# Kernel optimization log

Measured on AMD Instinct MI355X. Metric: run time of the kernel, lower is better.

Reference implementation:

```python
import jax, jax.numpy as jnp
import numpy as np

NEG_INF = -1000000000.0
B, N, D, H, L, DFF = 4, 1024, 512, 8, 6, 2048
DH = D // H
R2 = 10.0 ** 2  # locality_radius^2
EPS = 1e-5


def setup_inputs() -> dict:
    key = jax.random.key(0)
    ks = jax.random.split(key, 16)
    s = 0.02
    inp = {
        "tokens": jax.random.normal(ks[0], (B, N, D), jnp.float32),
        "xy": jax.random.uniform(ks[1], (B, N, 2), jnp.float32) * 100.0,
        "Wq": jax.random.normal(ks[2], (L, D, D), jnp.float32) * s,
        "Wk": jax.random.normal(ks[3], (L, D, D), jnp.float32) * s,
        "Wv": jax.random.normal(ks[4], (L, D, D), jnp.float32) * s,
        "Wo": jax.random.normal(ks[5], (L, D, D), jnp.float32) * s,
        "bo": jnp.zeros((L, D), jnp.float32),
        "W1": jax.random.normal(ks[6], (L, D, DFF), jnp.float32) * s,
        "b1": jnp.zeros((L, DFF), jnp.float32),
        "W2": jax.random.normal(ks[7], (L, DFF, D), jnp.float32) * s,
        "b2": jnp.zeros((L, D), jnp.float32),
        "g1": jnp.ones((L, D), jnp.float32),
        "be1": jnp.zeros((L, D), jnp.float32),
        "g2": jnp.ones((L, D), jnp.float32),
        "be2": jnp.zeros((L, D), jnp.float32),
        "gf": jnp.ones((D,), jnp.float32),
        "bf": jnp.zeros((D,), jnp.float32),
        "alive": jax.random.randint(ks[8], (B, N), 0, 2, dtype=jnp.int32),
        "species": jax.random.randint(ks[9], (B, N), 0, 3, dtype=jnp.int32),
        "n_agents": 512,
    }
    return inp


def _ln(x, g, b):
    m = jnp.mean(x, axis=-1, keepdims=True)
    v = jnp.mean((x - m) ** 2, axis=-1, keepdims=True)
    return (x - m) * jax.lax.rsqrt(v + EPS) * g + b


def _build_bias(alive, xy, species, dtype):
    # (B,1,N,N) additive bias, broadcast over heads (original repeats per head)
    af = alive.astype(dtype)
    bias = (1.0 - af)[:, None, None, :] * NEG_INF  # dead keys
    d2 = jnp.sum((xy[:, :, None, :] - xy[:, None, :, :]) ** 2, axis=-1)  # (B,N,N)
    bias = bias + jnp.where(d2 > R2, NEG_INF, 0.0)[:, None, :, :]
    ia = species < 2
    ip = species == 2
    ct = (ia[:, :, None] & ip[:, None, :]) | (ip[:, :, None] & ia[:, None, :])
    bias = bias + jnp.where(ct, NEG_INF, 0.0)[:, None, :, :]
    return bias


def reference(tokens, xy, Wq, Wk, Wv, Wo, bo, W1, b1, W2, b2,
              g1, be1, g2, be2, gf, bf, alive, species, n_agents):
    bias = _build_bias(alive, xy, species, tokens.dtype)
    scale = np.float32(np.sqrt(DH))
    x = tokens
    for l in range(L):
        h = _ln(x, g1[l], be1[l])
        q = (h @ Wq[l]).reshape(B, N, H, DH)
        k = (h @ Wk[l]).reshape(B, N, H, DH)
        v = (h @ Wv[l]).reshape(B, N, H, DH)
        scores = jnp.einsum('bihd,bjhd->bhij', q, k) / scale + bias
        w = jax.nn.softmax(scores, axis=-1)
        o = jnp.einsum('bhij,bjhd->bihd', w, v).reshape(B, N, D)
        x = x + (o @ Wo[l] + bo[l])
        h2 = _ln(x, g2[l], be2[l])
        ff = jax.nn.gelu(h2 @ W1[l] + b1[l], approximate=False) @ W2[l] + b2[l]
        x = x + ff
    return _ln(x, gf, bf)
```

## Files before the change

kernel.cpp:

```cpp
#include <hip/hip_runtime.h>
#include <math.h>

namespace {

constexpr int B = 4, N = 1024, D = 512, H = 8, DHd = 64, L = 6, DFFd = 2048;
constexpr int M = B * N;
constexpr int QKVS = 3 * D;
constexpr float NEG = -1000000000.0f;
constexpr float R2c = 100.0f;

typedef __attribute__((ext_vector_type(8))) short bf16x8;
typedef __attribute__((ext_vector_type(4))) float f32x4;
typedef __attribute__((ext_vector_type(16))) float f32x16;

__device__ __forceinline__ short f2bf(float f) {
  union { float f; unsigned u; } c; c.f = f;
  unsigned r = (c.u + 0x7fffu + ((c.u >> 16) & 1u)) >> 16;
  return (short)r;
}

__device__ __forceinline__ float gelu_f(float x) {
  return 0.5f * x * (1.0f + erff(x * 0.70710678118654752f));
}

__global__ __launch_bounds__(256) void bias_kernel(
    const float* __restrict__ xy, const int* __restrict__ alive,
    const int* __restrict__ species, float* __restrict__ bias)
{
  int j = blockIdx.x * 256 + threadIdx.x;
  int i = blockIdx.y;
  int b = blockIdx.z;
  float xi = xy[((size_t)b * N + i) * 2 + 0];
  float yi = xy[((size_t)b * N + i) * 2 + 1];
  float xj = xy[((size_t)b * N + j) * 2 + 0];
  float yj = xy[((size_t)b * N + j) * 2 + 1];
  float dx = xi - xj, dy = yi - yj;
  float d2 = dx * dx + dy * dy;
  float bv = 0.0f;
  if (alive[b * N + j] == 0) bv += NEG;
  if (d2 > R2c) bv += NEG;
  int si = species[b * N + i], sj = species[b * N + j];
  bool ia = si < 2, ip = si == 2, ja = sj < 2, jp = sj == 2;
  if ((ia && jp) || (ip && ja)) bv += NEG;
  bias[((size_t)b * N + i) * N + j] = bv;
}

__global__ __launch_bounds__(256) void wprep_kernel(
    const float* __restrict__ src, short* __restrict__ dst,
    int K, int Nc, size_t srcLS, size_t dstLS)
{
  __shared__ float t[32][33];
  int k0 = blockIdx.x * 32, n0 = blockIdx.y * 32;
  src += (size_t)blockIdx.z * srcLS;
  dst += (size_t)blockIdx.z * dstLS;
  int r = threadIdx.x >> 5, c = threadIdx.x & 31;
#pragma unroll
  for (int i = 0; i < 4; ++i)
    t[r + i * 8][c] = src[(size_t)(k0 + r + i * 8) * Nc + n0 + c];
  __syncthreads();
#pragma unroll
  for (int i = 0; i < 4; ++i)
    dst[(size_t)(n0 + r + i * 8) * K + k0 + c] = f2bf(t[c][r + i * 8]);
}

__global__ __launch_bounds__(64) void ln_kernel(
    const float* __restrict__ x, const float* __restrict__ g,
    const float* __restrict__ be, float* __restrict__ outf,
    short* __restrict__ outb)
{
  int row = blockIdx.x;
  int tid = threadIdx.x;
  const float* xr = x + (size_t)row * D;
  float v[8];
  float sum = 0.f;
#pragma unroll
  for (int i = 0; i < 8; ++i) { v[i] = xr[tid + i * 64]; sum += v[i]; }
#pragma unroll
  for (int off = 32; off > 0; off >>= 1) sum += __shfl_down(sum, off);
  sum = __shfl(sum, 0);
  float mean = sum * (1.0f / D);
  float vs = 0.f;
#pragma unroll
  for (int i = 0; i < 8; ++i) { float d = v[i] - mean; vs += d * d; }
#pragma unroll
  for (int off = 32; off > 0; off >>= 1) vs += __shfl_down(vs, off);
  vs = __shfl(vs, 0);
  float rstd = rsqrtf(vs * (1.0f / D) + 1e-5f);
#pragma unroll
  for (int i = 0; i < 8; ++i) {
    int c = tid + i * 64;
    float o = (v[i] - mean) * rstd * g[c] + be[c];
    if (outb) outb[(size_t)row * D + c] = f2bf(o);
    else      outf[(size_t)row * D + c] = o;
  }
}

__global__ __launch_bounds__(256, 2) void gemm_sk_kernel(
    const short* __restrict__ A, const short* __restrict__ Bt,
    const float* __restrict__ bvec, float* __restrict__ Cf,
    short* __restrict__ Cb, int K, int Nc, int mode)
{
  __shared__ __align__(16) char smem[4 * 17408];
  const int bm = blockIdx.y * 64, bn = blockIdx.x * 64;
  const int t = threadIdx.x, wave = t >> 6, lane = t & 63;
  const int half = lane >> 5;
  const int l32 = lane & 31;
  const int srow4 = lane >> 2, sseg4 = lane & 3;

  char* slot = smem + wave * 17408;
  const int kw0 = wave * (K >> 2);
  const int nch = K >> 7;

  const short* Ab = A + (size_t)(bm + srow4) * K + kw0 + sseg4 * 8;
  const short* Bb = Bt + (size_t)(bn + srow4) * K + kw0 + sseg4 * 8;

  auto issue = [&](int p, int kc) {
    char* ab = slot + p * 8192;
    char* bb = slot + p * 8192 + 4096;
#pragma unroll
    for (int i = 0; i < 4; ++i) {
      __builtin_amdgcn_global_load_lds(
          (const __attribute__((address_space(1))) void*)(Ab + (size_t)i * 16 * K + kc),
          (__attribute__((address_space(3))) void*)(ab + i * 1024), 16, 0, 0);
    }
#pragma unroll
    for (int i = 0; i < 4; ++i) {
      __builtin_amdgcn_global_load_lds(
          (const __attribute__((address_space(1))) void*)(Bb + (size_t)i * 16 * K + kc),
          (__attribute__((address_space(3))) void*)(bb + i * 1024), 16, 0, 0);
    }
  };

  f32x16 acc[2][2];
#pragma unroll
  for (int i = 0; i < 2; ++i)
#pragma unroll
    for (int j = 0; j < 2; ++j)
#pragma unroll
      for (int r = 0; r < 16; ++r) acc[i][j][r] = 0.f;

  issue(0, 0);
  for (int c = 0; c < nch; ++c) {
    const int p = c & 1;
    if (c + 1 < nch) {
      issue(p ^ 1, (c + 1) * 32);
      asm volatile("s_waitcnt vmcnt(%0)" :: "i"(8) : "memory");
    } else {
      asm volatile("s_waitcnt vmcnt(0)" ::: "memory");
    }
    const short* As = (const short*)(slot + p * 8192);
    const short* Bs = (const short*)(slot + p * 8192 + 4096);
#pragma unroll
    for (int ks = 0; ks < 2; ++ks) {
      bf16x8 a0 = *(const bf16x8*)&As[(l32) * 32 + ks * 16 + half * 8];
      bf16x8 a1 = *(const bf16x8*)&As[(32 + l32) * 32 + ks * 16 + half * 8];
      bf16x8 b0 = *(const bf16x8*)&Bs[(l32) * 32 + ks * 16 + half * 8];
      bf16x8 b1 = *(const bf16x8*)&Bs[(32 + l32) * 32 + ks * 16 + half * 8];
      acc[0][0] = __builtin_amdgcn_mfma_f32_32x32x16_bf16(a0, b0, acc[0][0], 0, 0, 0);
      acc[0][1] = __builtin_amdgcn_mfma_f32_32x32x16_bf16(a0, b1, acc[0][1], 0, 0, 0);
      acc[1][0] = __builtin_amdgcn_mfma_f32_32x32x16_bf16(a1, b0, acc[1][0], 0, 0, 0);
      acc[1][1] = __builtin_amdgcn_mfma_f32_32x32x16_bf16(a1, b1, acc[1][1], 0, 0, 0);
    }
  }

  float* red = (float*)slot;
#pragma unroll
  for (int ti = 0; ti < 2; ++ti)
#pragma unroll
    for (int tj = 0; tj < 2; ++tj)
#pragma unroll
      for (int r = 0; r < 16; ++r) {
        int row = ti * 32 + (r & 3) + 8 * (r >> 2) + 4 * half;
        red[row * 68 + tj * 32 + l32] = acc[ti][tj][r];
      }
  __syncthreads();

  const int row = t >> 2, cs = (t & 3) * 16;
  const size_t orow = (size_t)(bm + row) * Nc + bn + cs;
#pragma unroll
  for (int u = 0; u < 4; ++u) {
    float4 s0 = *(const float4*)((const float*)(smem + 0 * 17408) + row * 68 + cs + u * 4);
    float4 s1 = *(const float4*)((const float*)(smem + 1 * 17408) + row * 68 + cs + u * 4);
    float4 s2 = *(const float4*)((const float*)(smem + 2 * 17408) + row * 68 + cs + u * 4);
    float4 s3 = *(const float4*)((const float*)(smem + 3 * 17408) + row * 68 + cs + u * 4);
    float o0 = s0.x + s1.x + s2.x + s3.x;
    float o1 = s0.y + s1.y + s2.y + s3.y;
    float o2 = s0.z + s1.z + s2.z + s3.z;
    float o3 = s0.w + s1.w + s2.w + s3.w;
    const int col = bn + cs + u * 4;
    if (mode == 0) {
      short4 w = {f2bf(o0), f2bf(o1), f2bf(o2), f2bf(o3)};
      *(short4*)&Cb[orow + u * 4] = w;
    } else if (mode == 1) {
      float4 bv = *(const float4*)&bvec[col];
      float4 rv = *(const float4*)&Cf[orow + u * 4];
      float4 w = {o0 + bv.x + rv.x, o1 + bv.y + rv.y, o2 + bv.z + rv.z, o3 + bv.w + rv.w};
      *(float4*)&Cf[orow + u * 4] = w;
    } else {
      float4 bv = *(const float4*)&bvec[col];
      short4 w = {f2bf(gelu_f(o0 + bv.x)), f2bf(gelu_f(o1 + bv.y)),
                  f2bf(gelu_f(o2 + bv.z)), f2bf(gelu_f(o3 + bv.w))};
      *(short4*)&Cb[orow + u * 4] = w;
    }
  }
}

__global__ __launch_bounds__(256) void attn_mfma_kernel(
    const short* __restrict__ qkv, const float* __restrict__ bias,
    short* __restrict__ o)
{
  constexpr int LDR = 72;
  __shared__ __align__(16) short Qs[64 * LDR];
  __shared__ __align__(16) short Ks[2][64 * LDR];
  __shared__ __align__(16) short Vt[2][64 * LDR];
  __shared__ __align__(16) short Ps[4 * 16 * LDR];

  const int q0 = blockIdx.x * 64;
  const int hh = blockIdx.y;
  const int b  = blockIdx.z;
  const int t  = threadIdx.x;
  const int wave = t >> 6;
  const int lane = t & 63;
  const int quad = lane >> 4;
  const int ln16 = lane & 15;
  const int srow = t >> 2, sseg = t & 3;

  {
    const short* qb = qkv + (size_t)(b * N + q0 + srow) * QKVS + hh * 64 + sseg * 16;
    *(bf16x8*)&Qs[srow * LDR + sseg * 16] = *(const bf16x8*)qb;
    *(bf16x8*)&Qs[srow * LDR + sseg * 16 + 8] = *(const bf16x8*)(qb + 8);
  }
  __syncthreads();

  const int qrow = wave * 16 + ln16;
  const bf16x8 qf0 = *(const bf16x8*)&Qs[qrow * LDR + quad * 8];
  const bf16x8 qf1 = *(const bf16x8*)&Qs[qrow * LDR + 32 + quad * 8];

  float m_run = -1e30f, l_run = 0.f;
  f32x4 Oacc[4];
#pragma unroll
  for (int dt = 0; dt < 4; ++dt) Oacc[dt] = (f32x4){0.f, 0.f, 0.f, 0.f};

  short* Psw = Ps + wave * 16 * LDR;
  const float* brow = bias + (size_t)(b * N + q0 + wave * 16 + ln16) * N;
  const short* kb0 = qkv + (size_t)b * N * QKVS + 512 + hh * 64 + sseg * 16;
  const short* vb0 = qkv + (size_t)b * N * QKVS + 1024 + hh * 64 + sseg * 16;

  bf16x8 k0r = *(const bf16x8*)(kb0 + (size_t)srow * QKVS);
  bf16x8 k1r = *(const bf16x8*)(kb0 + (size_t)srow * QKVS + 8);
  bf16x8 v0r = *(const bf16x8*)(vb0 + (size_t)srow * QKVS);
  bf16x8 v1r = *(const bf16x8*)(vb0 + (size_t)srow * QKVS + 8);
  float4 b4[4];
#pragma unroll
  for (int ks = 0; ks < 4; ++ks)
    b4[ks] = *(const float4*)&brow[ks * 16 + quad * 4];

  for (int kt = 0; kt < 16; ++kt) {
    const int p = kt & 1;
    *(bf16x8*)&Ks[p][srow * LDR + sseg * 16] = k0r;
    *(bf16x8*)&Ks[p][srow * LDR + sseg * 16 + 8] = k1r;
#pragma unroll
    for (int e = 0; e < 8; ++e) {
      Vt[p][(sseg * 16 + e) * LDR + srow] = v0r[e];
      Vt[p][(sseg * 16 + 8 + e) * LDR + srow] = v1r[e];
    }
    const int k0n = (kt + 1 < 16) ? (kt + 1) * 64 : 0;
    bf16x8 nk0 = *(const bf16x8*)(kb0 + (size_t)(k0n + srow) * QKVS);
    bf16x8 nk1 = *(const bf16x8*)(kb0 + (size_t)(k0n + srow) * QKVS + 8);
    bf16x8 nv0 = *(const bf16x8*)(vb0 + (size_t)(k0n + srow) * QKVS);
    bf16x8 nv1 = *(const bf16x8*)(vb0 + (size_t)(k0n + srow) * QKVS + 8);
    float4 bcur[4] = {b4[0], b4[1], b4[2], b4[3]};
#pragma unroll
    for (int ks = 0; ks < 4; ++ks)
      b4[ks] = *(const float4*)&brow[k0n + ks * 16 + quad * 4];
    asm volatile("s_waitcnt lgkmcnt(0)\n\ts_barrier" ::: "memory");

    float sv[4][4];
#pragma unroll
    for (int ks = 0; ks < 4; ++ks) {
      bf16x8 a0 = *(const bf16x8*)&Ks[p][(ks * 16 + ln16) * LDR + quad * 8];
      bf16x8 a1 = *(const bf16x8*)&Ks[p][(ks * 16 + ln16) * LDR + 32 + quad * 8];
      f32x4 z = (f32x4){0.f, 0.f, 0.f, 0.f};
      z = __builtin_amdgcn_mfma_f32_16x16x32_bf16(a0, qf0, z, 0, 0, 0);
      z = __builtin_amdgcn_mfma_f32_16x16x32_bf16(a1, qf1, z, 0, 0, 0);
#pragma unroll
      for (int r = 0; r < 4; ++r)
        sv[ks][r] = z[r] * 0.125f + (&bcur[ks].x)[r];
    }

    float mt = sv[0][0];
#pragma unroll
    for (int ks = 0; ks < 4; ++ks)
#pragma unroll
      for (int r = 0; r < 4; ++r) mt = fmaxf(mt, sv[ks][r]);
    mt = fmaxf(mt, __shfl_xor(mt, 16));
    mt = fmaxf(mt, __shfl_xor(mt, 32));
    const float m_new = fmaxf(m_run, mt);
    const float alpha = __expf(m_run - m_new);
    m_run = m_new;
    float rs = 0.f;
    float pv[4][4];
#pragma unroll
    for (int ks = 0; ks < 4; ++ks)
#pragma unroll
      for (int r = 0; r < 4; ++r) {
        float e = __expf(sv[ks][r] - m_new);
        pv[ks][r] = e;
        rs += e;
      }
    rs += __shfl_xor(rs, 16);
    rs += __shfl_xor(rs, 32);
    l_run = l_run * alpha + rs;
    float af[4];
#pragma unroll
    for (int r = 0; r < 4; ++r) af[r] = __shfl(alpha, quad * 4 + r);
#pragma unroll
    for (int dt = 0; dt < 4; ++dt)
#pragma unroll
      for (int r = 0; r < 4; ++r) Oacc[dt][r] *= af[r];

#pragma unroll
    for (int ks = 0; ks < 4; ++ks) {
      short4 pk = {f2bf(pv[ks][0]), f2bf(pv[ks][1]), f2bf(pv[ks][2]), f2bf(pv[ks][3])};
      *(short4*)&Psw[ln16 * LDR + ks * 16 + quad * 4] = pk;
    }

    bf16x8 ap0 = *(const bf16x8*)&Psw[ln16 * LDR + quad * 8];
    bf16x8 ap1 = *(const bf16x8*)&Psw[ln16 * LDR + 32 + quad * 8];
#pragma unroll
    for (int dt = 0; dt < 4; ++dt) {
      bf16x8 bv0 = *(const bf16x8*)&Vt[p][(dt * 16 + ln16) * LDR + quad * 8];
      bf16x8 bv1 = *(const bf16x8*)&Vt[p][(dt * 16 + ln16) * LDR + 32 + quad * 8];
      Oacc[dt] = __builtin_amdgcn_mfma_f32_16x16x32_bf16(ap0, bv0, Oacc[dt], 0, 0, 0);
      Oacc[dt] = __builtin_amdgcn_mfma_f32_16x16x32_bf16(ap1, bv1, Oacc[dt], 0, 0, 0);
    }

    k0r = nk0; k1r = nk1; v0r = nv0; v1r = nv1;
  }

  const float linv = 1.0f / l_run;
  float iv[4];
#pragma unroll
  for (int r = 0; r < 4; ++r) iv[r] = __shfl(linv, quad * 4 + r);
#pragma unroll
  for (int dt = 0; dt < 4; ++dt) {
#pragma unroll
    for (int r = 0; r < 4; ++r) {
      int row = q0 + wave * 16 + quad * 4 + r;
      o[(size_t)(b * N + row) * D + hh * 64 + dt * 16 + ln16] =
          f2bf(Oacc[dt][r] * iv[r]);
    }
  }
}

}

extern "C" void kernel_launch(void* const* d_in, const int* in_sizes, int n_in,
                              void* d_out, int out_size, void* d_ws, size_t ws_size,
                              hipStream_t stream)
{
  const float* tokens  = (const float*)d_in[0];
  const float* xy      = (const float*)d_in[1];
  const float* Wq      = (const float*)d_in[2];
  const float* Wk      = (const float*)d_in[3];
  const float* Wv      = (const float*)d_in[4];
  const float* Wo      = (const float*)d_in[5];
  const float* bo      = (const float*)d_in[6];
  const float* W1      = (const float*)d_in[7];
  const float* b1      = (const float*)d_in[8];
  const float* W2      = (const float*)d_in[9];
  const float* b2      = (const float*)d_in[10];
  const float* g1      = (const float*)d_in[11];
  const float* be1     = (const float*)d_in[12];
  const float* g2      = (const float*)d_in[13];
  const float* be2     = (const float*)d_in[14];
  const float* gf      = (const float*)d_in[15];
  const float* bf      = (const float*)d_in[16];
  const int*   alive   = (const int*)d_in[17];
  const int*   species = (const int*)d_in[18];

  char* p = (char*)d_ws;
  float* bias = (float*)p; p += (size_t)B * N * N * 4;
  float* x    = (float*)p; p += (size_t)M * D * 4;
  short* h    = (short*)p; p += (size_t)M * D * 2;
  short* qkv  = (short*)p; p += (size_t)M * DFFd * 2;
  short* ff   = qkv;
  short* Wqkvt = (short*)p; p += (size_t)L * QKVS * D * 2;
  short* Wot   = (short*)p; p += (size_t)L * D * D * 2;
  short* W1t   = (short*)p; p += (size_t)L * DFFd * D * 2;
  short* W2t   = (short*)p; p += (size_t)L * D * DFFd * 2;

  hipMemcpyAsync(x, tokens, sizeof(float) * (size_t)M * D,
                 hipMemcpyDeviceToDevice, stream);
  bias_kernel<<<dim3(N / 256, N, B), 256, 0, stream>>>(xy, alive, species, bias);

  wprep_kernel<<<dim3(16, 16, L), 256, 0, stream>>>(
      Wq, Wqkvt + (size_t)0 * D * D, D, D, (size_t)D * D, (size_t)QKVS * D);
  wprep_kernel<<<dim3(16, 16, L), 256, 0, stream>>>(
      Wk, Wqkvt + (size_t)1 * D * D, D, D, (size_t)D * D, (size_t)QKVS * D);
  wprep_kernel<<<dim3(16, 16, L), 256, 0, stream>>>(
      Wv, Wqkvt + (size_t)2 * D * D, D, D, (size_t)D * D, (size_t)QKVS * D);
  wprep_kernel<<<dim3(16, 16, L), 256, 0, stream>>>(
      Wo, Wot, D, D, (size_t)D * D, (size_t)D * D);
  wprep_kernel<<<dim3(16, 64, L), 256, 0, stream>>>(
      W1, W1t, D, DFFd, (size_t)D * DFFd, (size_t)DFFd * D);
  wprep_kernel<<<dim3(64, 16, L), 256, 0, stream>>>(
      W2, W2t, DFFd, D, (size_t)DFFd * D, (size_t)D * DFFd);

  for (int l = 0; l < L; ++l) {
    ln_kernel<<<M, 64, 0, stream>>>(x, g1 + l * D, be1 + l * D, nullptr, h);
    gemm_sk_kernel<<<dim3(QKVS / 64, M / 64), 256, 0, stream>>>(
        h, Wqkvt + (size_t)l * QKVS * D, nullptr, nullptr, qkv, D, QKVS, 0);
    attn_mfma_kernel<<<dim3(N / 64, H, B), 256, 0, stream>>>(qkv, bias, h);
    gemm_sk_kernel<<<dim3(D / 64, M / 64), 256, 0, stream>>>(
        h, Wot + (size_t)l * D * D, bo + l * D, x, nullptr, D, D, 1);
    ln_kernel<<<M, 64, 0, stream>>>(x, g2 + l * D, be2 + l * D, nullptr, h);
    gemm_sk_kernel<<<dim3(DFFd / 64, M / 64), 256, 0, stream>>>(
        h, W1t + (size_t)l * DFFd * D, b1 + l * DFFd, nullptr, ff, D, DFFd, 2);
    gemm_sk_kernel<<<dim3(D / 64, M / 64), 256, 0, stream>>>(
        ff, W2t + (size_t)l * D * DFFd, b2 + l * D, x, nullptr, DFFd, D, 1);
  }
  ln_kernel<<<M, 64, 0, stream>>>(x, gf, bf, (float*)d_out, nullptr);
}
```

Baseline: 992.3 us.

## Replace intra-block split-K GEMM with 128x128 tiled GEMM and atomic grid split-K

The GEMM kernel changes from 64x64 tiles, where four waves each handle a quarter of K and reduce through shared memory, to 128x128 tiles where the four waves share double-buffered A/B tiles and each owns a 64x64 output quadrant. Each element of A and B is now reused across more outputs, and the shared-memory reduction pass goes away. Accumulator results are written straight from registers with bias, residual or GELU fused in. The N=512 GEMMs split K across grid z and combine with float atomicAdd to keep enough blocks in flight. This adds block-wide barriers on every chunk, uncoalesced scalar stores and atomic contention, and the atomic summation order is no longer deterministic.

```diff
diff --git a/kernel.cpp b/kernel.cpp
--- a/kernel.cpp
+++ b/kernel.cpp
@@ -95,40 +95,38 @@
   }
 }
 
-__global__ __launch_bounds__(256, 2) void gemm_sk_kernel(
+__global__ __launch_bounds__(256, 3) void gemm128_kernel(
     const short* __restrict__ A, const short* __restrict__ Bt,
     const float* __restrict__ bvec, float* __restrict__ Cf,
-    short* __restrict__ Cb, int K, int Nc, int mode)
-{
-  __shared__ __align__(16) char smem[4 * 17408];
-  const int bm = blockIdx.y * 64, bn = blockIdx.x * 64;
+    short* __restrict__ Cb, int K, int Nc, int mode, int nkz)
+{
+  __shared__ __align__(16) short As[2][4096];
+  __shared__ __align__(16) short Bs[2][4096];
+  const int bm = blockIdx.y * 128, bn = blockIdx.x * 128;
+  const int kz = blockIdx.z;
   const int t = threadIdx.x, wave = t >> 6, lane = t & 63;
-  const int half = lane >> 5;
-  const int l32 = lane & 31;
-  const int srow4 = lane >> 2, sseg4 = lane & 3;
-
-  char* slot = smem + wave * 17408;
-  const int kw0 = wave * (K >> 2);
-  const int nch = K >> 7;
-
-  const short* Ab = A + (size_t)(bm + srow4) * K + kw0 + sseg4 * 8;
-  const short* Bb = Bt + (size_t)(bn + srow4) * K + kw0 + sseg4 * 8;
+  const int wr = wave >> 1, wc = wave & 1;
+  const int l32 = lane & 31, half = lane >> 5;
+  const int Kz = K / nkz;
+  const int kw0 = kz * Kz;
+  const int nch = Kz >> 5;
+
+  const short* Ab = A  + (size_t)(bm + wave * 32 + (lane >> 2)) * K + kw0 + (lane & 3) * 8;
+  const short* Bb = Bt + (size_t)(bn + wave * 32 + (lane >> 2)) * K + kw0 + (lane & 3) * 8;
+  char* Abase = (char*)&As[0][0] + wave * 2048;
+  char* Bbase = (char*)&Bs[0][0] + wave * 2048;
 
   auto issue = [&](int p, int kc) {
-    char* ab = slot + p * 8192;
-    char* bb = slot + p * 8192 + 4096;
-#pragma unroll
-    for (int i = 0; i < 4; ++i) {
+#pragma unroll
+    for (int i = 0; i < 2; ++i)
       __builtin_amdgcn_global_load_lds(
           (const __attribute__((address_space(1))) void*)(Ab + (size_t)i * 16 * K + kc),
-          (__attribute__((address_space(3))) void*)(ab + i * 1024), 16, 0, 0);
-    }
-#pragma unroll
-    for (int i = 0; i < 4; ++i) {
+          (__attribute__((address_space(3))) void*)(Abase + p * 8192 + i * 1024), 16, 0, 0);
+#pragma unroll
+    for (int i = 0; i < 2; ++i)
       __builtin_amdgcn_global_load_lds(
           (const __attribute__((address_space(1))) void*)(Bb + (size_t)i * 16 * K + kc),
-          (__attribute__((address_space(3))) void*)(bb + i * 1024), 16, 0, 0);
-    }
+          (__attribute__((address_space(3))) void*)(Bbase + p * 8192 + i * 1024), 16, 0, 0);
   };
 
   f32x16 acc[2][2];
@@ -144,65 +142,53 @@
     const int p = c & 1;
     if (c + 1 < nch) {
       issue(p ^ 1, (c + 1) * 32);
-      asm volatile("s_waitcnt vmcnt(%0)" :: "i"(8) : "memory");
+      asm volatile("s_waitcnt vmcnt(%0)" :: "i"(4) : "memory");
     } else {
       asm volatile("s_waitcnt vmcnt(0)" ::: "memory");
     }
-    const short* As = (const short*)(slot + p * 8192);
-    const short* Bs = (const short*)(slot + p * 8192 + 4096);
+    __syncthreads();
+    const short* Ap = &As[p][0];
+    const short* Bp = &Bs[p][0];
 #pragma unroll
     for (int ks = 0; ks < 2; ++ks) {
-      bf16x8 a0 = *(const bf16x8*)&As[(l32) * 32 + ks * 16 + half * 8];
-      bf16x8 a1 = *(const bf16x8*)&As[(32 + l32) * 32 + ks * 16 + half * 8];
-      bf16x8 b0 = *(const bf16x8*)&Bs[(l32) * 32 + ks * 16 + half * 8];
-      bf16x8 b1 = *(const bf16x8*)&Bs[(32 + l32) * 32 + ks * 16 + half * 8];
+      bf16x8 a0 = *(const bf16x8*)&Ap[(wr * 64 + l32) * 32 + ks * 16 + half * 8];
+      bf16x8 a1 = *(const bf16x8*)&Ap[(wr * 64 + 32 + l32) * 32 + ks * 16 + half * 8];
+      bf16x8 b0 = *(const bf16x8*)&Bp[(wc * 64 + l32) * 32 + ks * 16 + half * 8];
+      bf16x8 b1 = *(const bf16x8*)&Bp[(wc * 64 + 32 + l32) * 32 + ks * 16 + half * 8];
       acc[0][0] = __builtin_amdgcn_mfma_f32_32x32x16_bf16(a0, b0, acc[0][0], 0, 0, 0);
       acc[0][1] = __builtin_amdgcn_mfma_f32_32x32x16_bf16(a0, b1, acc[0][1], 0, 0, 0);
       acc[1][0] = __builtin_amdgcn_mfma_f32_32x32x16_bf16(a1, b0, acc[1][0], 0, 0, 0);
       acc[1][1] = __builtin_amdgcn_mfma_f32_32x32x16_bf16(a1, b1, acc[1][1], 0, 0, 0);
     }
-  }
-
-  float* red = (float*)slot;
+    if (c + 1 < nch) __syncthreads();
+  }
+
+  float bv0 = 0.f, bv1 = 0.f;
+  if (mode == 2 || (mode == 1 && kz == 0)) {
+    bv0 = bvec[bn + wc * 64 + l32];
+    bv1 = bvec[bn + wc * 64 + 32 + l32];
+  }
 #pragma unroll
   for (int ti = 0; ti < 2; ++ti)
 #pragma unroll
-    for (int tj = 0; tj < 2; ++tj)
+    for (int tj = 0; tj < 2; ++tj) {
+      const float vb = tj ? bv1 : bv0;
 #pragma unroll
       for (int r = 0; r < 16; ++r) {
-        int row = ti * 32 + (r & 3) + 8 * (r >> 2) + 4 * half;
-        red[row * 68 + tj * 32 + l32] = acc[ti][tj][r];
+        const int row = bm + wr * 64 + ti * 32 + (r & 3) + 8 * (r >> 2) + 4 * half;
+        const int col = bn + wc * 64 + tj * 32 + l32;
+        const size_t idx = (size_t)row * Nc + col;
+        const float v = acc[ti][tj][r];
+        if (mode == 0) {
+          Cb[idx] = f2bf(v);
+        } else if (mode == 1) {
+          if (nkz == 1) Cf[idx] += v + vb;
+          else          atomicAdd(&Cf[idx], v + vb);
+        } else {
+          Cb[idx] = f2bf(gelu_f(v + vb));
+        }
       }
-  __syncthreads();
-
-  const int row = t >> 2, cs = (t & 3) * 16;
-  const size_t orow = (size_t)(bm + row) * Nc + bn + cs;
-#pragma unroll
-  for (int u = 0; u < 4; ++u) {
-    float4 s0 = *(const float4*)((const float*)(smem + 0 * 17408) + row * 68 + cs + u * 4);
-    float4 s1 = *(const float4*)((const float*)(smem + 1 * 17408) + row * 68 + cs + u * 4);
-    float4 s2 = *(const float4*)((const float*)(smem + 2 * 17408) + row * 68 + cs + u * 4);
-    float4 s3 = *(const float4*)((const float*)(smem + 3 * 17408) + row * 68 + cs + u * 4);
-    float o0 = s0.x + s1.x + s2.x + s3.x;
-    float o1 = s0.y + s1.y + s2.y + s3.y;
-    float o2 = s0.z + s1.z + s2.z + s3.z;
-    float o3 = s0.w + s1.w + s2.w + s3.w;
-    const int col = bn + cs + u * 4;
-    if (mode == 0) {
-      short4 w = {f2bf(o0), f2bf(o1), f2bf(o2), f2bf(o3)};
-      *(short4*)&Cb[orow + u * 4] = w;
-    } else if (mode == 1) {
-      float4 bv = *(const float4*)&bvec[col];
-      float4 rv = *(const float4*)&Cf[orow + u * 4];
-      float4 w = {o0 + bv.x + rv.x, o1 + bv.y + rv.y, o2 + bv.z + rv.z, o3 + bv.w + rv.w};
-      *(float4*)&Cf[orow + u * 4] = w;
-    } else {
-      float4 bv = *(const float4*)&bvec[col];
-      short4 w = {f2bf(gelu_f(o0 + bv.x)), f2bf(gelu_f(o1 + bv.y)),
-                  f2bf(gelu_f(o2 + bv.z)), f2bf(gelu_f(o3 + bv.w))};
-      *(short4*)&Cb[orow + u * 4] = w;
-    }
-  }
+    }
 }
 
 __global__ __launch_bounds__(256) void attn_mfma_kernel(
@@ -409,16 +395,16 @@
 
   for (int l = 0; l < L; ++l) {
     ln_kernel<<<M, 64, 0, stream>>>(x, g1 + l * D, be1 + l * D, nullptr, h);
-    gemm_sk_kernel<<<dim3(QKVS / 64, M / 64), 256, 0, stream>>>(
-        h, Wqkvt + (size_t)l * QKVS * D, nullptr, nullptr, qkv, D, QKVS, 0);
+    gemm128_kernel<<<dim3(QKVS / 128, M / 128, 1), 256, 0, stream>>>(
+        h, Wqkvt + (size_t)l * QKVS * D, nullptr, nullptr, qkv, D, QKVS, 0, 1);
     attn_mfma_kernel<<<dim3(N / 64, H, B), 256, 0, stream>>>(qkv, bias, h);
-    gemm_sk_kernel<<<dim3(D / 64, M / 64), 256, 0, stream>>>(
-        h, Wot + (size_t)l * D * D, bo + l * D, x, nullptr, D, D, 1);
+    gemm128_kernel<<<dim3(D / 128, M / 128, 2), 256, 0, stream>>>(
+        h, Wot + (size_t)l * D * D, bo + l * D, x, nullptr, D, D, 1, 2);
     ln_kernel<<<M, 64, 0, stream>>>(x, g2 + l * D, be2 + l * D, nullptr, h);
-    gemm_sk_kernel<<<dim3(DFFd / 64, M / 64), 256, 0, stream>>>(
-        h, W1t + (size_t)l * DFFd * D, b1 + l * DFFd, nullptr, ff, D, DFFd, 2);
-    gemm_sk_kernel<<<dim3(D / 64, M / 64), 256, 0, stream>>>(
-        ff, W2t + (size_t)l * D * DFFd, b2 + l * D, x, nullptr, DFFd, D, 1);
+    gemm128_kernel<<<dim3(DFFd / 128, M / 128, 1), 256, 0, stream>>>(
+        h, W1t + (size_t)l * DFFd * D, b1 + l * DFFd, nullptr, ff, D, DFFd, 2, 1);
+    gemm128_kernel<<<dim3(D / 128, M / 128, 2), 256, 0, stream>>>(
+        ff, W2t + (size_t)l * D * DFFd, b2 + l * D, x, nullptr, DFFd, D, 1, 2);
   }
   ln_kernel<<<M, 64, 0, stream>>>(x, gf, bf, (float*)d_out, nullptr);
 }
```

Result: slower. 1.223 ms (+23.2%).

## Fuse LayerNorm into QKV/FFN1 GEMMs, merge prep kernels, swizzle LDS tiles

Applied to the files above, without the earlier changes.

Adds a GEMM kernel that computes per-row LayerNorm statistics itself and normalises fp32 activations into bf16 LDS tiles on the fly. This removes the two separate LN launches per layer and the bf16 round trip of the normalised activations. All weight transposes, the bias mask build and the token copy are merged into a single prep launch. The GEMM LDS layout gets an XOR swizzle to cut bank conflicts, and the final LN packs four rows per block. In exchange, each of the 24 or 32 column blocks per row tile recomputes the row statistics and re-reads fp32 X, which adds redundant traffic.

```diff
diff --git a/kernel.cpp b/kernel.cpp
--- a/kernel.cpp
+++ b/kernel.cpp
@@ -3,7 +3,7 @@
 
 namespace {
 
-constexpr int B = 4, N = 1024, D = 512, H = 8, DHd = 64, L = 6, DFFd = 2048;
+constexpr int B = 4, N = 1024, D = 512, H = 8, L = 6, DFFd = 2048;
 constexpr int M = B * N;
 constexpr int QKVS = 3 * D;
 constexpr float NEG = -1000000000.0f;
@@ -23,53 +23,78 @@
   return 0.5f * x * (1.0f + erff(x * 0.70710678118654752f));
 }
 
-__global__ __launch_bounds__(256) void bias_kernel(
+__global__ __launch_bounds__(256) void prep_kernel(
+    const float* __restrict__ Wq, const float* __restrict__ Wk,
+    const float* __restrict__ Wv, const float* __restrict__ Wo,
+    const float* __restrict__ W1, const float* __restrict__ W2,
+    short* __restrict__ Wqkvt, short* __restrict__ Wot,
+    short* __restrict__ W1t, short* __restrict__ W2t,
     const float* __restrict__ xy, const int* __restrict__ alive,
-    const int* __restrict__ species, float* __restrict__ bias)
+    const int* __restrict__ species, float* __restrict__ bias,
+    const float* __restrict__ tokens, float* __restrict__ x)
 {
-  int j = blockIdx.x * 256 + threadIdx.x;
-  int i = blockIdx.y;
-  int b = blockIdx.z;
-  float xi = xy[((size_t)b * N + i) * 2 + 0];
-  float yi = xy[((size_t)b * N + i) * 2 + 1];
-  float xj = xy[((size_t)b * N + j) * 2 + 0];
-  float yj = xy[((size_t)b * N + j) * 2 + 1];
-  float dx = xi - xj, dy = yi - yj;
-  float d2 = dx * dx + dy * dy;
-  float bv = 0.0f;
-  if (alive[b * N + j] == 0) bv += NEG;
-  if (d2 > R2c) bv += NEG;
-  int si = species[b * N + i], sj = species[b * N + j];
-  bool ia = si < 2, ip = si == 2, ja = sj < 2, jp = sj == 2;
-  if ((ia && jp) || (ip && ja)) bv += NEG;
-  bias[((size_t)b * N + i) * N + j] = bv;
-}
-
-__global__ __launch_bounds__(256) void wprep_kernel(
-    const float* __restrict__ src, short* __restrict__ dst,
-    int K, int Nc, size_t srcLS, size_t dstLS)
+  __shared__ float tt[32][33];
+  const int blk = blockIdx.x;
+  const int t = threadIdx.x;
+
+  if (blk < 18432) {
+    const float* src; short* dst; int K, Nc, tx; size_t srcLS, dstLS; int lb;
+    if (blk < 6144) {
+      const int w = blk / 1536; lb = blk % 1536; tx = 16; K = 512; Nc = 512;
+      srcLS = (size_t)D * D;
+      if (w == 0)      { src = Wq; dst = Wqkvt; dstLS = (size_t)QKVS * D; }
+      else if (w == 1) { src = Wk; dst = Wqkvt + (size_t)D * D; dstLS = (size_t)QKVS * D; }
+      else if (w == 2) { src = Wv; dst = Wqkvt + (size_t)2 * D * D; dstLS = (size_t)QKVS * D; }
+      else             { src = Wo; dst = Wot; dstLS = (size_t)D * D; }
+    } else if (blk < 12288) {
+      lb = blk - 6144; tx = 16; K = 512; Nc = DFFd;
+      src = W1; dst = W1t; srcLS = (size_t)D * DFFd; dstLS = (size_t)DFFd * D;
+    } else {
+      lb = blk - 12288; tx = 64; K = DFFd; Nc = 512;
+      src = W2; dst = W2t; srcLS = (size_t)DFFd * D; dstLS = (size_t)D * DFFd;
+    }
+    const int per = (K / 32) * (Nc / 32);
+    const int z = lb / per, rem = lb % per;
+    const int k0 = (rem % tx) * 32, n0 = (rem / tx) * 32;
+    src += (size_t)z * srcLS; dst += (size_t)z * dstLS;
+    const int r = t >> 5, c = t & 31;
+#pragma unroll
+    for (int i = 0; i < 4; ++i)
+      tt[r + i * 8][c] = src[(size_t)(k0 + r + i * 8) * Nc + n0 + c];
+    __syncthreads();
+#pragma unroll
+    for (int i = 0; i < 4; ++i)
+      dst[(size_t)(n0 + r + i * 8) * K + k0 + c] = f2bf(tt[c][r + i * 8]);
+  } else if (blk < 34816) {
+    const int e = blk - 18432;
+    const int j = (e & 3) * 256 + t;
+    const int i = (e >> 2) & 1023;
+    const int b = e >> 12;
+    float xi = xy[((size_t)b * N + i) * 2 + 0];
+    float yi = xy[((size_t)b * N + i) * 2 + 1];
+    float xj = xy[((size_t)b * N + j) * 2 + 0];
+    float yj = xy[((size_t)b * N + j) * 2 + 1];
+    float dx = xi - xj, dy = yi - yj;
+    float d2 = dx * dx + dy * dy;
+    float bv = 0.0f;
+    if (alive[b * N + j] == 0) bv += NEG;
+    if (d2 > R2c) bv += NEG;
+    int si = species[b * N + i], sj = species[b * N + j];
+    bool ia = si < 2, ip = si == 2, ja = sj < 2, jp = sj == 2;
+    if ((ia && jp) || (ip && ja)) bv += NEG;
+    bias[((size_t)b * N + i) * N + j] = bv;
+  } else {
+    const size_t e = (size_t)(blk - 34816) * 256 + t;
+    ((float4*)x)[e] = ((const float4*)tokens)[e];
+  }
+}
+
+__global__ __launch_bounds__(256) void ln_kernel(
+    const float* __restrict__ x, const float* __restrict__ g,
+    const float* __restrict__ be, float* __restrict__ outf)
 {
-  __shared__ float t[32][33];
-  int k0 = blockIdx.x * 32, n0 = blockIdx.y * 32;
-  src += (size_t)blockIdx.z * srcLS;
-  dst += (size_t)blockIdx.z * dstLS;
-  int r = threadIdx.x >> 5, c = threadIdx.x & 31;
-#pragma unroll
-  for (int i = 0; i < 4; ++i)
-    t[r + i * 8][c] = src[(size_t)(k0 + r + i * 8) * Nc + n0 + c];
-  __syncthreads();
-#pragma unroll
-  for (int i = 0; i < 4; ++i)
-    dst[(size_t)(n0 + r + i * 8) * K + k0 + c] = f2bf(t[c][r + i * 8]);
-}
-
-__global__ __launch_bounds__(64) void ln_kernel(
-    const float* __restrict__ x, const float* __restrict__ g,
-    const float* __restrict__ be, float* __restrict__ outf,
-    short* __restrict__ outb)
-{
-  int row = blockIdx.x;
-  int tid = threadIdx.x;
+  int row = blockIdx.x * 4 + (threadIdx.x >> 6);
+  int tid = threadIdx.x & 63;
   const float* xr = x + (size_t)row * D;
   float v[8];
   float sum = 0.f;
@@ -89,9 +114,7 @@
 #pragma unroll
   for (int i = 0; i < 8; ++i) {
     int c = tid + i * 64;
-    float o = (v[i] - mean) * rstd * g[c] + be[c];
-    if (outb) outb[(size_t)row * D + c] = f2bf(o);
-    else      outf[(size_t)row * D + c] = o;
+    outf[(size_t)row * D + c] = (v[i] - mean) * rstd * g[c] + be[c];
   }
 }
 
@@ -105,7 +128,8 @@
   const int t = threadIdx.x, wave = t >> 6, lane = t & 63;
   const int half = lane >> 5;
   const int l32 = lane & 31;
-  const int srow4 = lane >> 2, sseg4 = lane & 3;
+  const int srow4 = lane >> 2;
+  const int sseg4 = (lane & 3) ^ ((lane >> 3) & 3);
 
   char* slot = smem + wave * 17408;
   const int kw0 = wave * (K >> 2);
@@ -118,18 +142,21 @@
     char* ab = slot + p * 8192;
     char* bb = slot + p * 8192 + 4096;
 #pragma unroll
-    for (int i = 0; i < 4; ++i) {
+    for (int i = 0; i < 4; ++i)
       __builtin_amdgcn_global_load_lds(
           (const __attribute__((address_space(1))) void*)(Ab + (size_t)i * 16 * K + kc),
           (__attribute__((address_space(3))) void*)(ab + i * 1024), 16, 0, 0);
-    }
-#pragma unroll
-    for (int i = 0; i < 4; ++i) {
+#pragma unroll
+    for (int i = 0; i < 4; ++i)
       __builtin_amdgcn_global_load_lds(
           (const __attribute__((address_space(1))) void*)(Bb + (size_t)i * 16 * K + kc),
           (__attribute__((address_space(3))) void*)(bb + i * 1024), 16, 0, 0);
-    }
   };
+
+  const int key = (l32 >> 1) & 3;
+  int offs[2];
+#pragma unroll
+  for (int ks = 0; ks < 2; ++ks) offs[ks] = ((ks * 2 + half) ^ key) * 8;
 
   f32x16 acc[2][2];
 #pragma unroll
@@ -144,7 +171,7 @@
     const int p = c & 1;
     if (c + 1 < nch) {
       issue(p ^ 1, (c + 1) * 32);
-      asm volatile("s_waitcnt vmcnt(%0)" :: "i"(8) : "memory");
+      asm volatile("s_waitcnt vmcnt(8)" ::: "memory");
     } else {
       asm volatile("s_waitcnt vmcnt(0)" ::: "memory");
     }
@@ -152,10 +179,10 @@
     const short* Bs = (const short*)(slot + p * 8192 + 4096);
 #pragma unroll
     for (int ks = 0; ks < 2; ++ks) {
-      bf16x8 a0 = *(const bf16x8*)&As[(l32) * 32 + ks * 16 + half * 8];
-      bf16x8 a1 = *(const bf16x8*)&As[(32 + l32) * 32 + ks * 16 + half * 8];
-      bf16x8 b0 = *(const bf16x8*)&Bs[(l32) * 32 + ks * 16 + half * 8];
-      bf16x8 b1 = *(const bf16x8*)&Bs[(32 + l32) * 32 + ks * 16 + half * 8];
+      bf16x8 a0 = *(const bf16x8*)&As[(l32) * 32 + offs[ks]];
+      bf16x8 a1 = *(const bf16x8*)&As[(32 + l32) * 32 + offs[ks]];
+      bf16x8 b0 = *(const bf16x8*)&Bs[(l32) * 32 + offs[ks]];
+      bf16x8 b1 = *(const bf16x8*)&Bs[(32 + l32) * 32 + offs[ks]];
       acc[0][0] = __builtin_amdgcn_mfma_f32_32x32x16_bf16(a0, b0, acc[0][0], 0, 0, 0);
       acc[0][1] = __builtin_amdgcn_mfma_f32_32x32x16_bf16(a0, b1, acc[0][1], 0, 0, 0);
       acc[1][0] = __builtin_amdgcn_mfma_f32_32x32x16_bf16(a1, b0, acc[1][0], 0, 0, 0);
@@ -205,6 +232,166 @@
   }
 }
 
+__global__ __launch_bounds__(256, 2) void gemm_skln_kernel(
+    const float* __restrict__ X, const short* __restrict__ Bt,
+    const float* __restrict__ g, const float* __restrict__ be,
+    const float* __restrict__ bvec, short* __restrict__ Cb,
+    int Nc, int mode)
+{
+  __shared__ __align__(16) char smem[4 * 17408];
+  __shared__ float s_mean[64], s_rstd[64];
+  __shared__ float s_g[512], s_be[512];
+  const int bm = blockIdx.y * 64, bn = blockIdx.x * 64;
+  const int t = threadIdx.x, wave = t >> 6, lane = t & 63;
+  const int half = lane >> 5, l32 = lane & 31;
+
+  s_g[t] = g[t]; s_g[t + 256] = g[t + 256];
+  s_be[t] = be[t]; s_be[t + 256] = be[t + 256];
+
+  {
+    const float* xr = X + (size_t)(bm + (t >> 2)) * 512 + (t & 3) * 128;
+    float s1 = 0.f, s2 = 0.f;
+#pragma unroll
+    for (int i = 0; i < 32; ++i) {
+      float4 v = *(const float4*)(xr + i * 4);
+      s1 += v.x + v.y + v.z + v.w;
+      s2 += v.x * v.x + v.y * v.y + v.z * v.z + v.w * v.w;
+    }
+    s1 += __shfl_xor(s1, 1); s1 += __shfl_xor(s1, 2);
+    s2 += __shfl_xor(s2, 1); s2 += __shfl_xor(s2, 2);
+    if ((t & 3) == 0) {
+      float mn = s1 * (1.f / 512.f);
+      float var = s2 * (1.f / 512.f) - mn * mn;
+      s_mean[t >> 2] = mn;
+      s_rstd[t >> 2] = rsqrtf(var + 1e-5f);
+    }
+  }
+  __syncthreads();
+
+  char* slot = smem + wave * 17408;
+  const int kw0 = wave * 128;
+  const int srow4 = lane >> 2;
+  const int sseg4 = (lane & 3) ^ ((lane >> 3) & 3);
+  const short* Bb = Bt + (size_t)(bn + srow4) * 512 + kw0 + sseg4 * 8;
+
+  auto issueB = [&](int p, int c) {
+    char* bb = slot + p * 8192 + 4096;
+#pragma unroll
+    for (int i = 0; i < 4; ++i)
+      __builtin_amdgcn_global_load_lds(
+          (const __attribute__((address_space(1))) void*)(Bb + (size_t)i * 16 * 512 + c * 32),
+          (__attribute__((address_space(3))) void*)(bb + i * 1024), 16, 0, 0);
+  };
+
+  float4 areg[8];
+  auto issueA = [&](int c) {
+    const int k0 = kw0 + c * 32;
+#pragma unroll
+    for (int j = 0; j < 8; ++j) {
+      const int row = (j >> 1) * 16 + (lane >> 2);
+      const int col = (j & 1) * 16 + (lane & 3) * 4;
+      areg[j] = *(const float4*)(X + (size_t)(bm + row) * 512 + k0 + col);
+    }
+  };
+  auto writeA = [&](int c, int p) {
+    const int k0 = kw0 + c * 32;
+    short* As = (short*)(slot + p * 8192);
+#pragma unroll
+    for (int j = 0; j < 8; ++j) {
+      const int row = (j >> 1) * 16 + (lane >> 2);
+      const int col = (j & 1) * 16 + (lane & 3) * 4;
+      const float mn = s_mean[row], rs = s_rstd[row];
+      float o0 = (areg[j].x - mn) * rs * s_g[k0 + col + 0] + s_be[k0 + col + 0];
+      float o1 = (areg[j].y - mn) * rs * s_g[k0 + col + 1] + s_be[k0 + col + 1];
+      float o2 = (areg[j].z - mn) * rs * s_g[k0 + col + 2] + s_be[k0 + col + 2];
+      float o3 = (areg[j].w - mn) * rs * s_g[k0 + col + 3] + s_be[k0 + col + 3];
+      short4 w = {f2bf(o0), f2bf(o1), f2bf(o2), f2bf(o3)};
+      const int gl = col >> 3, sub = (col >> 2) & 1;
+      const int gs = gl ^ ((row >> 1) & 3);
+      *(short4*)&As[row * 32 + gs * 8 + sub * 4] = w;
+    }
+  };
+
+  const int key = (l32 >> 1) & 3;
+  int offs[2];
+#pragma unroll
+  for (int ks = 0; ks < 2; ++ks) offs[ks] = ((ks * 2 + half) ^ key) * 8;
+
+  f32x16 acc[2][2];
+#pragma unroll
+  for (int i = 0; i < 2; ++i)
+#pragma unroll
+    for (int j = 0; j < 2; ++j)
+#pragma unroll
+      for (int r = 0; r < 16; ++r) acc[i][j][r] = 0.f;
+
+  asm volatile("s_waitcnt vmcnt(0)" ::: "memory");
+  issueA(0); issueB(0, 0);
+  asm volatile("s_waitcnt vmcnt(4)" ::: "memory");
+  writeA(0, 0);
+  issueA(1); issueB(1, 1);
+#pragma unroll
+  for (int c = 0; c < 4; ++c) {
+    const int p = c & 1;
+    if (c < 3) asm volatile("s_waitcnt vmcnt(12)" ::: "memory");
+    else       asm volatile("s_waitcnt vmcnt(0)" ::: "memory");
+    const short* As = (const short*)(slot + p * 8192);
+    const short* Bs = (const short*)(slot + p * 8192 + 4096);
+#pragma unroll
+    for (int ks = 0; ks < 2; ++ks) {
+      bf16x8 a0 = *(const bf16x8*)&As[(l32) * 32 + offs[ks]];
+      bf16x8 a1 = *(const bf16x8*)&As[(32 + l32) * 32 + offs[ks]];
+      bf16x8 b0 = *(const bf16x8*)&Bs[(l32) * 32 + offs[ks]];
+      bf16x8 b1 = *(const bf16x8*)&Bs[(32 + l32) * 32 + offs[ks]];
+      acc[0][0] = __builtin_amdgcn_mfma_f32_32x32x16_bf16(a0, b0, acc[0][0], 0, 0, 0);
+      acc[0][1] = __builtin_amdgcn_mfma_f32_32x32x16_bf16(a0, b1, acc[0][1], 0, 0, 0);
+      acc[1][0] = __builtin_amdgcn_mfma_f32_32x32x16_bf16(a1, b0, acc[1][0], 0, 0, 0);
+      acc[1][1] = __builtin_amdgcn_mfma_f32_32x32x16_bf16(a1, b1, acc[1][1], 0, 0, 0);
+    }
+    if (c < 3) {
+      asm volatile("s_waitcnt vmcnt(4)" ::: "memory");
+      writeA(c + 1, p ^ 1);
+      if (c < 2) { issueA(c + 2); issueB(p, c + 2); }
+    }
+  }
+
+  float* red = (float*)slot;
+#pragma unroll
+  for (int ti = 0; ti < 2; ++ti)
+#pragma unroll
+    for (int tj = 0; tj < 2; ++tj)
+#pragma unroll
+      for (int r = 0; r < 16; ++r) {
+        int row = ti * 32 + (r & 3) + 8 * (r >> 2) + 4 * half;
+        red[row * 68 + tj * 32 + l32] = acc[ti][tj][r];
+      }
+  __syncthreads();
+
+  const int row = t >> 2, cs = (t & 3) * 16;
+  const size_t orow = (size_t)(bm + row) * Nc + bn + cs;
+#pragma unroll
+  for (int u = 0; u < 4; ++u) {
+    float4 s0 = *(const float4*)((const float*)(smem + 0 * 17408) + row * 68 + cs + u * 4);
+    float4 s1 = *(const float4*)((const float*)(smem + 1 * 17408) + row * 68 + cs + u * 4);
+    float4 s2 = *(const float4*)((const float*)(smem + 2 * 17408) + row * 68 + cs + u * 4);
+    float4 s3 = *(const float4*)((const float*)(smem + 3 * 17408) + row * 68 + cs + u * 4);
+    float o0 = s0.x + s1.x + s2.x + s3.x;
+    float o1 = s0.y + s1.y + s2.y + s3.y;
+    float o2 = s0.z + s1.z + s2.z + s3.z;
+    float o3 = s0.w + s1.w + s2.w + s3.w;
+    const int col = bn + cs + u * 4;
+    if (mode == 0) {
+      short4 w = {f2bf(o0), f2bf(o1), f2bf(o2), f2bf(o3)};
+      *(short4*)&Cb[orow + u * 4] = w;
+    } else {
+      float4 bv = *(const float4*)&bvec[col];
+      short4 w = {f2bf(gelu_f(o0 + bv.x)), f2bf(gelu_f(o1 + bv.y)),
+                  f2bf(gelu_f(o2 + bv.z)), f2bf(gelu_f(o3 + bv.w))};
+      *(short4*)&Cb[orow + u * 4] = w;
+    }
+  }
+}
+
 __global__ __launch_bounds__(256) void attn_mfma_kernel(
     const short* __restrict__ qkv, const float* __restrict__ bias,
     short* __restrict__ o)
@@ -390,35 +577,22 @@
   short* W1t   = (short*)p; p += (size_t)L * DFFd * D * 2;
   short* W2t   = (short*)p; p += (size_t)L * D * DFFd * 2;
 
-  hipMemcpyAsync(x, tokens, sizeof(float) * (size_t)M * D,
-                 hipMemcpyDeviceToDevice, stream);
-  bias_kernel<<<dim3(N / 256, N, B), 256, 0, stream>>>(xy, alive, species, bias);
-
-  wprep_kernel<<<dim3(16, 16, L), 256, 0, stream>>>(
-      Wq, Wqkvt + (size_t)0 * D * D, D, D, (size_t)D * D, (size_t)QKVS * D);
-  wprep_kernel<<<dim3(16, 16, L), 256, 0, stream>>>(
-      Wk, Wqkvt + (size_t)1 * D * D, D, D, (size_t)D * D, (size_t)QKVS * D);
-  wprep_kernel<<<dim3(16, 16, L), 256, 0, stream>>>(
-      Wv, Wqkvt + (size_t)2 * D * D, D, D, (size_t)D * D, (size_t)QKVS * D);
-  wprep_kernel<<<dim3(16, 16, L), 256, 0, stream>>>(
-      Wo, Wot, D, D, (size_t)D * D, (size_t)D * D);
-  wprep_kernel<<<dim3(16, 64, L), 256, 0, stream>>>(
-      W1, W1t, D, DFFd, (size_t)D * DFFd, (size_t)DFFd * D);
-  wprep_kernel<<<dim3(64, 16, L), 256, 0, stream>>>(
-      W2, W2t, DFFd, D, (size_t)DFFd * D, (size_t)D * DFFd);
+  prep_kernel<<<36864, 256, 0, stream>>>(
+      Wq, Wk, Wv, Wo, W1, W2, Wqkvt, Wot, W1t, W2t,
+      xy, alive, species, bias, tokens, x);
 
   for (int l = 0; l < L; ++l) {
-    ln_kernel<<<M, 64, 0, stream>>>(x, g1 + l * D, be1 + l * D, nullptr, h);
-    gemm_sk_kernel<<<dim3(QKVS / 64, M / 64), 256, 0, stream>>>(
-        h, Wqkvt + (size_t)l * QKVS * D, nullptr, nullptr, qkv, D, QKVS, 0);
+    gemm_skln_kernel<<<dim3(QKVS / 64, M / 64), 256, 0, stream>>>(
+        x, Wqkvt + (size_t)l * QKVS * D, g1 + l * D, be1 + l * D,
+        nullptr, qkv, QKVS, 0);
     attn_mfma_kernel<<<dim3(N / 64, H, B), 256, 0, stream>>>(qkv, bias, h);
     gemm_sk_kernel<<<dim3(D / 64, M / 64), 256, 0, stream>>>(
         h, Wot + (size_t)l * D * D, bo + l * D, x, nullptr, D, D, 1);
-    ln_kernel<<<M, 64, 0, stream>>>(x, g2 + l * D, be2 + l * D, nullptr, h);
-    gemm_sk_kernel<<<dim3(DFFd / 64, M / 64), 256, 0, stream>>>(
-        h, W1t + (size_t)l * DFFd * D, b1 + l * DFFd, nullptr, ff, D, DFFd, 2);
+    gemm_skln_kernel<<<dim3(DFFd / 64, M / 64), 256, 0, stream>>>(
+        x, W1t + (size_t)l * DFFd * D, g2 + l * D, be2 + l * D,
+        b1 + l * DFFd, ff, DFFd, 2);
     gemm_sk_kernel<<<dim3(D / 64, M / 64), 256, 0, stream>>>(
         ff, W2t + (size_t)l * D * DFFd, b2 + l * D, x, nullptr, DFFd, D, 1);
   }
-  ln_kernel<<<M, 64, 0, stream>>>(x, gf, bf, (float*)d_out, nullptr);
-}
+  ln_kernel<<<M / 4, 256, 0, stream>>>(x, gf, bf, (float*)d_out);
+}
```

After: 1.233 ms. 1.24x slower.
